# Kernel tuning notes

Measured on AMD Instinct MI355X. Metric: run time of the kernel, lower is better.

## Reference

```python
import jax, jax.numpy as jnp
import numpy as np

B, T = 128, 50
VOCAB, EMB_D, GRU_H = 10000, 200, 100
HEADS, AHID, THID = 8, 96, 96

def _conv(x, w, b, pad):
    y = jax.lax.conv_general_dilated(x, w, (1, 1), pad,
        dimension_numbers=('NCHW', 'OIHW', 'NCHW'))
    return y + b[None, :, None, None]

def _bn(x, g, b, m, v):
    s = jax.lax.rsqrt(v + 1e-5)
    return (x - m[None, :, None, None]) * (g * s)[None, :, None, None] + b[None, :, None, None]

def _maxpool(x):
    return jax.lax.reduce_window(x, -jnp.inf, jax.lax.max, (1, 1, 2, 2), (1, 1, 2, 2), 'VALID')

def _resize(x):
    # F.interpolate(mode='bilinear', align_corners=False) == half-pixel bilinear, no antialias
    return jax.image.resize(x, (x.shape[0], x.shape[1], 25, 156), 'bilinear', antialias=False)

def _audio_attn(x, wq, bq, wk, bk, wv, bv):
    # x: [B,96,H,W]; wq: [heads,96,96] == stacked per-head 1x1 convs
    Q = jnp.einsum('bchw,noc->bnohw', x, wq) + bq[None, :, :, None, None]
    K = jnp.einsum('bchw,noc->bnohw', x, wk) + bk[None, :, :, None, None]
    V = jnp.einsum('bchw,noc->bnohw', x, wv) + bv[None, :, :, None, None]
    # torch F.softmax with no dim on a 4D tensor defaults to dim=1 (channels) -> axis=2 here
    return jax.nn.softmax(Q * K, axis=2) * V  # [B,heads,96,H,W]

def _text_attn(o, wq, bq, wk, bk, wv, bv):
    # o: [N,100]; wq: [heads,96,100] == stacked per-head Linear layers
    Q = jnp.einsum('nd,hod->nho', o, wq) + bq[None]
    K = jnp.einsum('nd,hod->nho', o, wk) + bk[None]
    V = jnp.einsum('nd,hod->nho', o, wv) + bv[None]
    a = jax.nn.softmax(Q * K, axis=2) * V  # 2D softmax default dim=1 -> over feature axis
    return a.reshape(o.shape[0], -1)  # head-concat order == torch cat along dim=1

def _gru(xs, w_ih, w_hh, b_ih, b_hh):
    # xs: [T,B,200]; torch gate order r, z, n; b_hn applied inside r-gating
    def step(h, x):
        gi = x @ w_ih.T + b_ih
        gh = h @ w_hh.T + b_hh
        ir, iz, inew = jnp.split(gi, 3, axis=1)
        hr, hz, hnew = jnp.split(gh, 3, axis=1)
        r = jax.nn.sigmoid(ir + hr)
        z = jax.nn.sigmoid(iz + hz)
        n = jnp.tanh(inew + r * hnew)
        h2 = (1.0 - z) * n + z * h
        return h2, h2
    h0 = jnp.zeros((xs.shape[1], GRU_H), xs.dtype)
    hT, outs = jax.lax.scan(step, h0, xs)
    return outs, hT

def _forward(tokens, lengths, mfcc_t, mfcc_f, mfcc_c, w1a, b1a, g1a, be1a, m1a, v1a, w1b, b1b, g1b, be1b, m1b, v1b, w2, b2, g2, be2, m2, v2, w3, b3, g3, be3, m3, v3, w4, b4, g4, be4, m4, v4, wq_a1, bq_a1, wk_a1, bk_a1, wv_a1, bv_a1, wq_a2, bq_a2, wk_a2, bk_a2, wv_a2, bv_a2, emb, w_ih, w_hh, b_ih, b_hh, wq_t1, bq_t1, wk_t1, bk_t1, wv_t1, bv_t1, wq_t2, bq_t2, wk_t2, bk_t2, wv_t2, bv_t2, w_fa, b_fa, w_ft, b_ft, w_e, b_e):
    # --- audio CNN stem (eval-mode batchnorm; dropout off) ---
    xa = jax.nn.relu(_bn(_conv(mfcc_t, w1a, b1a, 'VALID'), g1a, be1a, m1a, v1a))
    xb = jax.nn.relu(_bn(_conv(mfcc_f, w1b, b1b, 'VALID'), g1b, be1b, m1b, v1b))
    # NOTE: original source reuses conv1b/bn1b for the third input (faithful to that)
    xc = jax.nn.relu(_bn(_conv(mfcc_c, w1b, b1b, 'VALID'), g1b, be1b, m1b, v1b))
    x = jnp.concatenate([_resize(xa), _resize(xb), _resize(xc)], axis=1)  # [B,24,25,156]
    x = _maxpool(jax.nn.relu(_bn(_conv(x, w2, b2, [(1, 1), (1, 1)]), g2, be2, m2, v2)))  # [B,32,12,78]
    x = _maxpool(jax.nn.relu(_bn(_conv(x, w3, b3, [(1, 1), (1, 1)]), g3, be3, m3, v3)))  # [B,64,6,39]
    x = jax.nn.relu(_bn(_conv(x, w4, b4, [(1, 1), (1, 1)]), g4, be4, m4, v4))            # [B,96,6,39]
    # --- two stacked per-head audio attentions, then per-head spatial GAP ---
    a1 = _audio_attn(x, wq_a1, bq_a1, wk_a1, bk_a1, wv_a1, bv_a1).mean(axis=(-2, -1))  # [B,8,96]
    a2 = _audio_attn(x, wq_a2, bq_a2, wk_a2, bk_a2, wv_a2, bv_a2).mean(axis=(-2, -1))
    # forward() slices heads along the height concat and GAPs -> per head [stage1 96, stage2 96]
    self_attn_audio = jnp.concatenate([a1, a2], axis=2).reshape(x.shape[0], -1)  # [B,1536]
    # --- text branch: embedding + GRU (all lengths == T -> pack/pad is identity) ---
    ex = jnp.swapaxes(emb[tokens], 0, 1)  # [T,B,200]
    outs, h = _gru(ex, w_ih, w_hh, b_ih, b_hh)  # h: [B,100]
    output = jnp.swapaxes(outs, 0, 1).reshape(-1, GRU_H)  # [B*T,100]
    t1 = _text_attn(output, wq_t1, bq_t1, wk_t1, bk_t1, wv_t1, bv_t1)
    t2 = _text_attn(output, wq_t2, bq_t2, wk_t2, bk_t2, wv_t2, bv_t2)
    self_attn_text = jnp.concatenate([t1, t2], axis=1).reshape(x.shape[0], T, -1).sum(axis=1)  # [B,1536]
    # --- cross-modal gated fusion ---
    x_gap = x.mean(axis=(-2, -1))  # [B,96]
    a_text = jax.nn.softmax(x_gap @ w_fa.T + b_fa, axis=1)   # [B,100]
    attn_text_based_audio = a_text * h                        # [B,100]
    a_audio = jax.nn.softmax(h @ w_ft.T + b_ft, axis=1)      # [B,96]
    attn_audio_based_text = a_audio * x_gap                   # [B,96]
    feat = jnp.concatenate([self_attn_audio, self_attn_text,
                            attn_audio_based_text, attn_text_based_audio], axis=1)  # [B,3268]
    return feat @ w_e.T + b_e  # [B,4] emotion logits

def setup_inputs() -> dict:
    key = jax.random.key(0)
    ks = iter(jax.random.split(key, 100))
    nrm = lambda s, sc=0.05: jax.random.normal(next(ks), s, jnp.float32) * sc
    uni = lambda s: jax.random.uniform(next(ks), s, jnp.float32) * 0.5 + 0.5
    d = {}
    d['mfcc_t'] = jax.random.normal(next(ks), (B, 1, 200, 40), jnp.float32)
    d['mfcc_f'] = jax.random.normal(next(ks), (B, 1, 200, 40), jnp.float32)
    d['mfcc_c'] = jax.random.normal(next(ks), (B, 1, 200, 40), jnp.float32)
    d['tokens'] = jax.random.randint(next(ks), (B, T), 0, VOCAB)
    d['lengths'] = jnp.full((B,), T, jnp.int32)
    def bnp(pre, c):
        d['g' + pre] = 1.0 + nrm((c,)); d['be' + pre] = nrm((c,))
        d['m' + pre] = nrm((c,)); d['v' + pre] = uni((c,))
    d['w1a'] = nrm((8, 1, 5, 2), 0.2); d['b1a'] = nrm((8,)); bnp('1a', 8)
    d['w1b'] = nrm((8, 1, 2, 6), 0.2); d['b1b'] = nrm((8,)); bnp('1b', 8)
    d['w2'] = nrm((32, 24, 3, 3), 0.1); d['b2'] = nrm((32,)); bnp('2', 32)
    d['w3'] = nrm((64, 32, 3, 3), 0.1); d['b3'] = nrm((64,)); bnp('3', 64)
    d['w4'] = nrm((96, 64, 3, 3), 0.08); d['b4'] = nrm((96,)); bnp('4', 96)
    for s in ('1', '2'):
        for p in ('q', 'k', 'v'):
            d['w%s_a%s' % (p, s)] = nrm((HEADS, 96, 96), 0.1)
            d['b%s_a%s' % (p, s)] = nrm((HEADS, 96))
    d['emb'] = nrm((VOCAB, EMB_D), 0.1)
    d['w_ih'] = nrm((3 * GRU_H, EMB_D), 0.1); d['w_hh'] = nrm((3 * GRU_H, GRU_H), 0.1)
    d['b_ih'] = nrm((3 * GRU_H,)); d['b_hh'] = nrm((3 * GRU_H,))
    for s in ('1', '2'):
        for p in ('q', 'k', 'v'):
            d['w%s_t%s' % (p, s)] = nrm((HEADS, THID, GRU_H), 0.1)
            d['b%s_t%s' % (p, s)] = nrm((HEADS, THID))
    d['w_fa'] = nrm((100, 96), 0.1); d['b_fa'] = nrm((100,))
    d['w_ft'] = nrm((96, 100), 0.1); d['b_ft'] = nrm((96,))
    d['w_e'] = nrm((4, 2 * HEADS * AHID + 2 * HEADS * THID + 96 + 100), 0.05); d['b_e'] = nrm((4,))
    return d

def reference(mfcc_t, mfcc_f, mfcc_c, tokens, lengths, w1a, b1a, g1a, be1a, m1a, v1a, w1b, b1b, g1b, be1b, m1b, v1b, w2, b2, g2, be2, m2, v2, w3, b3, g3, be3, m3, v3, w4, b4, g4, be4, m4, v4, wq_a1, bq_a1, wk_a1, bk_a1, wv_a1, bv_a1, wq_a2, bq_a2, wk_a2, bk_a2, wv_a2, bv_a2, emb, w_ih, w_hh, b_ih, b_hh, wq_t1, bq_t1, wk_t1, bk_t1, wv_t1, bv_t1, wq_t2, bq_t2, wk_t2, bk_t2, wv_t2, bv_t2, w_fa, b_fa, w_ft, b_ft, w_e, b_e):
    return _forward(tokens, lengths, mfcc_t, mfcc_f, mfcc_c, w1a, b1a, g1a, be1a, m1a, v1a, w1b, b1b, g1b, be1b, m1b, v1b, w2, b2, g2, be2, m2, v2, w3, b3, g3, be3, m3, v3, w4, b4, g4, be4, m4, v4, wq_a1, bq_a1, wk_a1, bk_a1, wv_a1, bv_a1, wq_a2, bq_a2, wk_a2, bk_a2, wv_a2, bv_a2, emb, w_ih, w_hh, b_ih, b_hh, wq_t1, bq_t1, wk_t1, bk_t1, wv_t1, bv_t1, wq_t2, bq_t2, wk_t2, bk_t2, wv_t2, bv_t2, w_fa, b_fa, w_ft, b_ft, w_e, b_e)
```

## Files before the change

kernel.cpp:

```cpp
#include <hip/hip_runtime.h>
#include <math.h>

static constexpr int kB = 128;
static constexpr int kT = 50;

struct TDesc { const float* src; float* dst; int O; int C; int total; };
struct TPack { TDesc d[15]; };
__global__ void k_transpose_pack(TPack p) {
    TDesc t = p.d[blockIdx.y];
    int idx = blockIdx.x * 256 + threadIdx.x;
    if (idx >= t.total) return;
    int o = idx % t.O; int r = idx / t.O; int c = r % t.C; int n = r / t.C;
    t.dst[idx] = t.src[((size_t)n * t.O + o) * t.C + c];
}

__global__ void k_zero(float* __restrict__ a, int n) {
    int i = blockIdx.x * 256 + threadIdx.x;
    if (i < n) a[i] = 0.f;
}

__global__ void k_stem(const float* __restrict__ mt, const float* __restrict__ mf,
                       const float* __restrict__ mc,
                       const float* __restrict__ w1a, const float* __restrict__ b1a,
                       const float* __restrict__ g1a, const float* __restrict__ be1a,
                       const float* __restrict__ m1a, const float* __restrict__ v1a,
                       const float* __restrict__ w1b, const float* __restrict__ b1b,
                       const float* __restrict__ g1b, const float* __restrict__ be1b,
                       const float* __restrict__ m1b, const float* __restrict__ v1b,
                       float* __restrict__ out, int total) {
    int idx = blockIdx.x * blockDim.x + threadIdx.x;
    if (idx >= total) return;
    int ox = idx % 156; int t = idx / 156;
    int oy = t % 25; t /= 25;
    int ch = t % 24; int b = t / 24;
    int grp = ch >> 3, c = ch & 7;
    const float* src; int Hc, Wc;
    const float *wb, *cb, *g, *be, *m, *v;
    if (grp == 0) { src = mt; Hc = 196; Wc = 39; wb = w1a + c * 10;
                    cb = b1a; g = g1a; be = be1a; m = m1a; v = v1a; }
    else          { src = (grp == 1 ? mf : mc); Hc = 199; Wc = 35; wb = w1b + c * 12;
                    cb = b1b; g = g1b; be = be1b; m = m1b; v = v1b; }
    float s = g[c] * rsqrtf(v[c] + 1e-5f);
    float bias = (cb[c] - m[c]) * s + be[c];
    float sy = (oy + 0.5f) * ((float)Hc / 25.f) - 0.5f;
    float sx = (ox + 0.5f) * ((float)Wc / 156.f) - 0.5f;
    float fy0 = floorf(sy), fx0 = floorf(sx);
    float fy = sy - fy0, fx = sx - fx0;
    int y0 = (int)fy0, x0 = (int)fx0;
    int y0c = min(max(y0, 0), Hc - 1), y1c = min(max(y0 + 1, 0), Hc - 1);
    int x0c = min(max(x0, 0), Wc - 1), x1c = min(max(x0 + 1, 0), Wc - 1);
    bool xs = (x1c == x0c), ys = (y1c == y0c);
    const float* p = src + (size_t)b * 8000;
    float t00, t01, t10, t11;
    if (grp == 0) {
        float W[6][3];
        #pragma unroll
        for (int r = 0; r < 6; ++r) {
            int rr = min(y0c + r, 199);
            #pragma unroll
            for (int cc = 0; cc < 3; ++cc)
                W[r][cc] = p[rr * 40 + min(x0c + cc, 39)];
        }
        float a00 = 0.f, a01 = 0.f, a10 = 0.f, a11 = 0.f;
        #pragma unroll
        for (int ky = 0; ky < 5; ++ky)
            #pragma unroll
            for (int kx = 0; kx < 2; ++kx) {
                float wv = wb[ky * 2 + kx];
                a00 += W[ky][kx] * wv;     a01 += W[ky][kx + 1] * wv;
                a10 += W[ky + 1][kx] * wv; a11 += W[ky + 1][kx + 1] * wv;
            }
        t00 = a00;
        t01 = xs ? a00 : a01;
        t10 = ys ? a00 : a10;
        t11 = xs ? (ys ? a00 : a10) : (ys ? a01 : a11);
    } else {
        float W[3][7];
        #pragma unroll
        for (int r = 0; r < 3; ++r) {
            int rr = min(y0c + r, 199);
            #pragma unroll
            for (int cc = 0; cc < 7; ++cc)
                W[r][cc] = p[rr * 40 + min(x0c + cc, 39)];
        }
        float a00 = 0.f, a01 = 0.f, a10 = 0.f, a11 = 0.f;
        #pragma unroll
        for (int ky = 0; ky < 2; ++ky)
            #pragma unroll
            for (int kx = 0; kx < 6; ++kx) {
                float wv = wb[ky * 6 + kx];
                a00 += W[ky][kx] * wv;     a01 += W[ky][kx + 1] * wv;
                a10 += W[ky + 1][kx] * wv; a11 += W[ky + 1][kx + 1] * wv;
            }
        t00 = a00;
        t01 = xs ? a00 : a01;
        t10 = ys ? a00 : a10;
        t11 = xs ? (ys ? a00 : a10) : (ys ? a01 : a11);
    }
    float r00 = fmaxf(t00 * s + bias, 0.f), r01 = fmaxf(t01 * s + bias, 0.f);
    float r10 = fmaxf(t10 * s + bias, 0.f), r11 = fmaxf(t11 * s + bias, 0.f);
    out[idx] = r00 * (1.f - fy) * (1.f - fx) + r01 * (1.f - fy) * fx
             + r10 * fy * (1.f - fx) + r11 * fy * fx;
}

template<int CIN, int CI_T, int H, int W, int ROWS, int NPX>
__global__ void __launch_bounds__(256) k_conv3x3_tiled(
    const float* __restrict__ in, const float* __restrict__ wT,
    const float* __restrict__ cb, const float* __restrict__ g,
    const float* __restrict__ be, const float* __restrict__ m,
    const float* __restrict__ v, float* __restrict__ out, int COUT) {
    constexpr int WP = W + 2;
    constexpr int RP = ROWS + 2;
    constexpr int STAGE = CI_T * RP * WP;
    __shared__ float sx[STAGE];
    __shared__ float sw[CI_T * 9 * 8];
    const int b = blockIdx.x, rt = blockIdx.y, oc0 = blockIdx.z * 8;
    const int row0 = rt * ROWS;
    const int tid = threadIdx.x;

    int off[NPX]; bool val[NPX];
    #pragma unroll
    for (int j = 0; j < NPX; ++j) {
        int px = tid + j * 256;
        int oy = px / W, ox = px - oy * W;
        bool ok = (px < ROWS * W) && (row0 + oy < H);
        val[j] = ok;
        off[j] = ok ? (oy * WP + ox) : 0;
    }

    float acc[NPX][8];
    #pragma unroll
    for (int j = 0; j < NPX; ++j)
        #pragma unroll
        for (int o = 0; o < 8; ++o) acc[j][o] = 0.f;

    for (int c0 = 0; c0 < CIN; c0 += CI_T) {
        __syncthreads();
        for (int e = tid; e < STAGE; e += 256) {
            int ci = e / (RP * WP);
            int rem = e - ci * RP * WP;
            int r = rem / WP;
            int xx = rem - r * WP;
            int iy = row0 - 1 + r;
            int ix = xx - 1;
            float vv = 0.f;
            if (iy >= 0 && iy < H && ix >= 0 && ix < W)
                vv = in[((size_t)(b * CIN + c0 + ci) * H + iy) * W + ix];
            sx[e] = vv;
        }
        for (int e = tid; e < CI_T * 9 * 8; e += 256) {
            int rk = e >> 3;
            int o = e & 7;
            sw[e] = wT[((size_t)c0 * 9 + rk) * COUT + oc0 + o];
        }
        __syncthreads();
        #pragma unroll 1
        for (int cl = 0; cl < CI_T; ++cl) {
            const float* sxc = sx + cl * RP * WP;
            #pragma unroll
            for (int k = 0; k < 9; ++k) {
                const int ky = k / 3, kx = k % 3;
                const float4 wa = *(const float4*)(sw + (cl * 9 + k) * 8);
                const float4 wb = *(const float4*)(sw + (cl * 9 + k) * 8 + 4);
                #pragma unroll
                for (int j = 0; j < NPX; ++j) {
                    float xv = sxc[off[j] + ky * WP + kx];
                    acc[j][0] += xv * wa.x; acc[j][1] += xv * wa.y;
                    acc[j][2] += xv * wa.z; acc[j][3] += xv * wa.w;
                    acc[j][4] += xv * wb.x; acc[j][5] += xv * wb.y;
                    acc[j][6] += xv * wb.z; acc[j][7] += xv * wb.w;
                }
            }
        }
    }
    float sc[8], bi[8];
    #pragma unroll
    for (int o = 0; o < 8; ++o) {
        float s = g[oc0 + o] * rsqrtf(v[oc0 + o] + 1e-5f);
        sc[o] = s; bi[o] = (cb[oc0 + o] - m[oc0 + o]) * s + be[oc0 + o];
    }
    #pragma unroll
    for (int j = 0; j < NPX; ++j) if (val[j]) {
        int px = tid + j * 256;
        int oy = row0 + px / W, ox = px % W;
        #pragma unroll
        for (int o = 0; o < 8; ++o)
            out[((size_t)(b * COUT + oc0 + o) * H + oy) * W + ox] =
                fmaxf(acc[j][o] * sc[o] + bi[o], 0.f);
    }
}

__global__ void k_maxpool(const float* __restrict__ in, float* __restrict__ out,
                          int C, int Hin, int Win, int Hout, int Wout, int total) {
    int idx = blockIdx.x * blockDim.x + threadIdx.x;
    if (idx >= total) return;
    int ox = idx % Wout; int t = idx / Wout;
    int oy = t % Hout; t /= Hout;
    int c = t % C; int b = t / C;
    const float* p = in + ((size_t)(b * C + c) * Hin + 2 * oy) * Win + 2 * ox;
    float m0 = fmaxf(p[0], p[1]);
    float m1 = fmaxf(p[Win], p[Win + 1]);
    out[idx] = fmaxf(m0, m1);
}

__global__ void __launch_bounds__(256) k_xgap(const float* __restrict__ x,
                                              float* __restrict__ xgap) {
    int b = blockIdx.x, tid = threadIdx.x;
    int wave = tid >> 6, lane = tid & 63;
    for (int c = wave; c < 96; c += 4) {
        const float* row = x + ((size_t)b * 96 + c) * 234;
        float s = 0.f;
        for (int p = lane; p < 234; p += 64) s += row[p];
        #pragma unroll
        for (int off = 1; off < 64; off <<= 1) s += __shfl_xor(s, off);
        if (lane == 0) xgap[b * 96 + c] = s * (1.f / 234.f);
    }
}

__global__ void __launch_bounds__(256, 2) k_audio_attn(
    const float* __restrict__ x,
    const float* __restrict__ wq1, const float* __restrict__ bq1,
    const float* __restrict__ wk1, const float* __restrict__ bk1,
    const float* __restrict__ wv1, const float* __restrict__ bv1,
    const float* __restrict__ wq2, const float* __restrict__ bq2,
    const float* __restrict__ wk2, const float* __restrict__ bk2,
    const float* __restrict__ wv2, const float* __restrict__ bv2,
    float* __restrict__ afeat) {
    const int b = blockIdx.x >> 1, pt = blockIdx.x & 1;
    const int n = blockIdx.y, stage = blockIdx.z;
    const float* wq = (stage ? wq2 : wq1) + n * 9216;
    const float* wk = (stage ? wk2 : wk1) + n * 9216;
    const float* wv = (stage ? wv2 : wv1) + n * 9216;
    const float* bqn = (stage ? bq2 : bq1) + n * 96;
    const float* bkn = (stage ? bk2 : bk1) + n * 96;
    const float* bvn = (stage ? bv2 : bv1) + n * 96;
    const int tid = threadIdx.x;
    const int to = tid >> 4, tpg = tid & 15;
    const int ob = to * 6;
    const int pA = tpg * 4;
    const int p0 = pt * 128;

    __shared__ float sxc[16 * 128];
    __shared__ float sw[4608];
    float* sred = sw;

    const float* xb = x + (size_t)b * (96 * 234) + p0;

    float qa[6][8], ka[6][8], va[6][8];
    #pragma unroll
    for (int j = 0; j < 6; ++j) {
        float bq_ = bqn[ob + j], bk_ = bkn[ob + j], bv_ = bvn[ob + j];
        #pragma unroll
        for (int i = 0; i < 8; ++i) { qa[j][i] = bq_; ka[j][i] = bk_; va[j][i] = bv_; }
    }

    for (int c0 = 0; c0 < 96; c0 += 16) {
        __syncthreads();
        {
            #pragma unroll
            for (int it = 0; it < 4; ++it) {
                int e2 = tid + it * 256;
                int r = e2 >> 6, c2 = (e2 & 63) * 2;
                float2 v = make_float2(0.f, 0.f);
                if (p0 + c2 < 234) v = *(const float2*)(xb + (c0 + r) * 234 + c2);
                *(float2*)(sxc + r * 128 + c2) = v;
            }
        }
        for (int e4 = tid; e4 < 1152; e4 += 256) {
            int mat = (e4 >= 768) ? 2 : (e4 >= 384 ? 1 : 0);
            int r4 = e4 - mat * 384;
            const float* wsrc = (mat == 0) ? wq : (mat == 1 ? wk : wv);
            *(float4*)(sw + mat * 1536 + r4 * 4) = *(const float4*)(wsrc + c0 * 96 + r4 * 4);
        }
        __syncthreads();
        #pragma unroll 2
        for (int cc = 0; cc < 16; ++cc) {
            float4 xa = *(const float4*)(sxc + cc * 128 + pA);
            float4 xc = *(const float4*)(sxc + cc * 128 + 64 + pA);
            const float* wr = sw + cc * 96 + ob;
            float2 q01 = *(const float2*)(wr);
            float2 q23 = *(const float2*)(wr + 2);
            float2 q45 = *(const float2*)(wr + 4);
            float2 k01 = *(const float2*)(wr + 1536);
            float2 k23 = *(const float2*)(wr + 1538);
            float2 k45 = *(const float2*)(wr + 1540);
            float2 v01 = *(const float2*)(wr + 3072);
            float2 v23 = *(const float2*)(wr + 3074);
            float2 v45 = *(const float2*)(wr + 3076);
            float wqv[6] = {q01.x, q01.y, q23.x, q23.y, q45.x, q45.y};
            float wkv[6] = {k01.x, k01.y, k23.x, k23.y, k45.x, k45.y};
            float wvv[6] = {v01.x, v01.y, v23.x, v23.y, v45.x, v45.y};
            #pragma unroll
            for (int j = 0; j < 6; ++j) {
                qa[j][0] += wqv[j] * xa.x; qa[j][1] += wqv[j] * xa.y;
                qa[j][2] += wqv[j] * xa.z; qa[j][3] += wqv[j] * xa.w;
                qa[j][4] += wqv[j] * xc.x; qa[j][5] += wqv[j] * xc.y;
                qa[j][6] += wqv[j] * xc.z; qa[j][7] += wqv[j] * xc.w;
                ka[j][0] += wkv[j] * xa.x; ka[j][1] += wkv[j] * xa.y;
                ka[j][2] += wkv[j] * xa.z; ka[j][3] += wkv[j] * xa.w;
                ka[j][4] += wkv[j] * xc.x; ka[j][5] += wkv[j] * xc.y;
                ka[j][6] += wkv[j] * xc.z; ka[j][7] += wkv[j] * xc.w;
                va[j][0] += wvv[j] * xa.x; va[j][1] += wvv[j] * xa.y;
                va[j][2] += wvv[j] * xa.z; va[j][3] += wvv[j] * xa.w;
                va[j][4] += wvv[j] * xc.x; va[j][5] += wvv[j] * xc.y;
                va[j][6] += wvv[j] * xc.z; va[j][7] += wvv[j] * xc.w;
            }
        }
    }

    int col[8];
    #pragma unroll
    for (int i = 0; i < 4; ++i) { col[i] = pA + i; col[4 + i] = 64 + pA + i; }

    float pmx[8];
    #pragma unroll
    for (int i = 0; i < 8; ++i) pmx[i] = -1e30f;
    #pragma unroll
    for (int j = 0; j < 6; ++j)
        #pragma unroll
        for (int i = 0; i < 8; ++i) {
            float sv = qa[j][i] * ka[j][i];
            qa[j][i] = sv;
            pmx[i] = fmaxf(pmx[i], sv);
        }
    __syncthreads();
    #pragma unroll
    for (int i = 0; i < 8; ++i) sred[to * 128 + col[i]] = pmx[i];
    __syncthreads();
    float m_[8];
    #pragma unroll
    for (int i = 0; i < 8; ++i) {
        float mm = -1e30f;
        for (int t = 0; t < 16; ++t) mm = fmaxf(mm, sred[t * 128 + col[i]]);
        m_[i] = mm;
    }
    __syncthreads();
    float z[8];
    #pragma unroll
    for (int i = 0; i < 8; ++i) z[i] = 0.f;
    #pragma unroll
    for (int j = 0; j < 6; ++j)
        #pragma unroll
        for (int i = 0; i < 8; ++i) {
            float e = __expf(qa[j][i] - m_[i]);
            qa[j][i] = e;
            z[i] += e;
        }
    #pragma unroll
    for (int i = 0; i < 8; ++i) sred[to * 128 + col[i]] = z[i];
    __syncthreads();
    float rz[8];
    #pragma unroll
    for (int i = 0; i < 8; ++i) {
        float zs = 0.f;
        for (int t = 0; t < 16; ++t) zs += sred[t * 128 + col[i]];
        rz[i] = (p0 + col[i] < 234) ? 1.f / zs : 0.f;
    }
    __syncthreads();
    #pragma unroll
    for (int j = 0; j < 6; ++j) {
        float po = 0.f;
        #pragma unroll
        for (int i = 0; i < 8; ++i) po += qa[j][i] * rz[i] * va[j][i];
        sred[(ob + j) * 16 + tpg] = po;
    }
    __syncthreads();
    if (tid < 96) {
        float ssum = 0.f;
        #pragma unroll
        for (int t = 0; t < 16; ++t) ssum += sred[tid * 16 + t];
        atomicAdd(afeat + b * 1536 + n * 192 + stage * 96 + tid, ssum * (1.f / 234.f));
    }
}

__global__ void __launch_bounds__(320) k_gi(const int* __restrict__ tokens,
        const float* __restrict__ emb, const float* __restrict__ w_ih,
        const float* __restrict__ b_ih, float* __restrict__ GI) {
    int r0 = blockIdx.x * 8;
    int tid = threadIdx.x;
    __shared__ float er[8][200];
    for (int e = tid; e < 1600; e += 320) {
        int r = e / 200, c = e - r * 200;
        er[r][c] = emb[(size_t)tokens[r0 + r] * 200 + c];
    }
    __syncthreads();
    if (tid < 300) {
        float acc[8];
        float bv = b_ih[tid];
        #pragma unroll
        for (int r = 0; r < 8; ++r) acc[r] = bv;
        for (int k4 = 0; k4 < 50; ++k4) {
            float4 w4 = *(const float4*)(w_ih + (size_t)tid * 200 + k4 * 4);
            #pragma unroll
            for (int r = 0; r < 8; ++r) {
                float4 x4 = *(const float4*)&er[r][k4 * 4];
                acc[r] += w4.x * x4.x + w4.y * x4.y + w4.z * x4.z + w4.w * x4.w;
            }
        }
        #pragma unroll
        for (int r = 0; r < 8; ++r)
            GI[(size_t)(r0 + r) * 300 + tid] = acc[r];
    }
}

__global__ void __launch_bounds__(320) k_gru_all(const float* __restrict__ GI,
        const float* __restrict__ w_hh, const float* __restrict__ b_hh,
        float* __restrict__ outs) {
    int b = blockIdx.x, tid = threadIdx.x;
    __shared__ float hs[100];
    __shared__ float gH[300];
    float4 wreg[25];
    float bias = 0.f;
    if (tid < 300) {
        bias = b_hh[tid];
        #pragma unroll
        for (int k4 = 0; k4 < 25; ++k4)
            wreg[k4] = *(const float4*)(w_hh + (size_t)tid * 100 + k4 * 4);
    }
    if (tid < 100) hs[tid] = 0.f;
    __syncthreads();
    for (int t = 0; t < kT; ++t) {
        if (tid < 300) {
            float gh = bias;
            #pragma unroll
            for (int k4 = 0; k4 < 25; ++k4) {
                float4 h4 = *(const float4*)&hs[k4 * 4];
                gh += wreg[k4].x * h4.x + wreg[k4].y * h4.y
                    + wreg[k4].z * h4.z + wreg[k4].w * h4.w;
            }
            gH[tid] = gh;
        }
        __syncthreads();
        if (tid < 100) {
            const float* gi = GI + ((size_t)b * kT + t) * 300;
            float r = 1.f / (1.f + expf(-(gi[tid] + gH[tid])));
            float z = 1.f / (1.f + expf(-(gi[100 + tid] + gH[100 + tid])));
            float nn = tanhf(gi[200 + tid] + r * gH[200 + tid]);
            float h2 = (1.f - z) * nn + z * hs[tid];
            hs[tid] = h2;
            outs[((size_t)b * kT + t) * 100 + tid] = h2;
        }
        __syncthreads();
    }
}

__global__ void __launch_bounds__(128) k_text_attn(const float* __restrict__ outs,
    const float* __restrict__ wq1, const float* __restrict__ bq1,
    const float* __restrict__ wk1, const float* __restrict__ bk1,
    const float* __restrict__ wv1, const float* __restrict__ bv1,
    const float* __restrict__ wq2, const float* __restrict__ bq2,
    const float* __restrict__ wk2, const float* __restrict__ bk2,
    const float* __restrict__ wv2, const float* __restrict__ bv2,
    float* __restrict__ tfeat) {
    int b = blockIdx.x, stage = blockIdx.y, n = blockIdx.z;
    const float* wq = stage ? wq2 : wq1; const float* bq = stage ? bq2 : bq1;
    const float* wk = stage ? wk2 : wk1; const float* bk = stage ? bk2 : bk1;
    const float* wv = stage ? wv2 : wv1; const float* bv = stage ? bv2 : bv1;
    int tid = threadIdx.x;
    bool act = tid < 96;
    int oo = act ? tid : 0;
    const float* wqc = wq + n * 9600 + oo;
    const float* wkc = wk + n * 9600 + oo;
    const float* wvc = wv + n * 9600 + oo;
    float bqv = act ? bq[n * 96 + tid] : 0.f;
    float bkv = act ? bk[n * 96 + tid] : 0.f;
    float bvv = act ? bv[n * 96 + tid] : 0.f;
    __shared__ float rows[10][100];
    __shared__ float wredM[2][10], wredS[2][10];
    float acc = 0.f;
    int wave = tid >> 6, lane = tid & 63;
    for (int tile = 0; tile < 5; ++tile) {
        int t0 = tile * 10;
        __syncthreads();
        for (int e = tid; e < 1000; e += 128) {
            int tt = e / 100, c = e - tt * 100;
            rows[tt][c] = outs[((size_t)b * kT + t0 + tt) * 100 + c];
        }
        __syncthreads();
        float q[10], k[10], v[10];
        #pragma unroll
        for (int tt = 0; tt < 10; ++tt) { q[tt] = bqv; k[tt] = bkv; v[tt] = bvv; }
        for (int c4 = 0; c4 < 25; ++c4) {
            int cb = c4 * 4 * 96;
            float q0 = wqc[cb], q1 = wqc[cb + 96], q2 = wqc[cb + 192], q3 = wqc[cb + 288];
            float k0 = wkc[cb], k1 = wkc[cb + 96], k2 = wkc[cb + 192], k3 = wkc[cb + 288];
            float v0 = wvc[cb], v1 = wvc[cb + 96], v2 = wvc[cb + 192], v3 = wvc[cb + 288];
            #pragma unroll
            for (int tt = 0; tt < 10; ++tt) {
                float4 x4 = *(const float4*)&rows[tt][c4 * 4];
                q[tt] += q0 * x4.x + q1 * x4.y + q2 * x4.z + q3 * x4.w;
                k[tt] += k0 * x4.x + k1 * x4.y + k2 * x4.z + k3 * x4.w;
                v[tt] += v0 * x4.x + v1 * x4.y + v2 * x4.z + v3 * x4.w;
            }
        }
        float s[10], e_[10];
        #pragma unroll
        for (int tt = 0; tt < 10; ++tt) s[tt] = act ? q[tt] * k[tt] : -1e30f;
        #pragma unroll
        for (int tt = 0; tt < 10; ++tt) {
            float m = s[tt];
            #pragma unroll
            for (int off = 1; off < 64; off <<= 1) m = fmaxf(m, __shfl_xor(m, off));
            if (lane == 0) wredM[wave][tt] = m;
        }
        __syncthreads();
        #pragma unroll
        for (int tt = 0; tt < 10; ++tt) {
            float mx = fmaxf(wredM[0][tt], wredM[1][tt]);
            e_[tt] = expf(s[tt] - mx);
        }
        #pragma unroll
        for (int tt = 0; tt < 10; ++tt) {
            float sm = e_[tt];
            #pragma unroll
            for (int off = 1; off < 64; off <<= 1) sm += __shfl_xor(sm, off);
            if (lane == 0) wredS[wave][tt] = sm;
        }
        __syncthreads();
        #pragma unroll
        for (int tt = 0; tt < 10; ++tt) {
            float sm = wredS[0][tt] + wredS[1][tt];
            acc += e_[tt] / sm * v[tt];
        }
    }
    if (act) tfeat[b * 1536 + stage * 768 + n * 96 + tid] = acc;
}

__global__ void __launch_bounds__(128) k_final(const float* __restrict__ xgap,
    const float* __restrict__ outs, const float* __restrict__ afeat,
    const float* __restrict__ tfeat,
    const float* __restrict__ w_fa, const float* __restrict__ b_fa,
    const float* __restrict__ w_ft, const float* __restrict__ b_ft,
    const float* __restrict__ w_e, const float* __restrict__ b_e,
    float* __restrict__ out) {
    int b = blockIdx.x; int tid = threadIdx.x;
    __shared__ float xg[96], hv[100], st[100], sa[96], aat[96], atba[100];
    __shared__ float redm[2], reds[2];
    if (tid < 96) xg[tid] = xgap[b * 96 + tid];
    if (tid < 100) hv[tid] = outs[(size_t)(b * kT + kT - 1) * 100 + tid];
    __syncthreads();
    if (tid < 100) {
        float acc = b_fa[tid];
        const float* wr = w_fa + tid * 96;
        for (int c = 0; c < 96; ++c) acc += wr[c] * xg[c];
        st[tid] = acc;
    }
    if (tid < 96) {
        float acc = b_ft[tid];
        const float* wr = w_ft + tid * 100;
        for (int c = 0; c < 100; ++c) acc += wr[c] * hv[c];
        sa[tid] = acc;
    }
    __syncthreads();
    if (tid == 0) {
        float mxv = -1e30f; for (int i = 0; i < 100; ++i) mxv = fmaxf(mxv, st[i]);
        float s = 0.f; for (int i = 0; i < 100; ++i) s += expf(st[i] - mxv);
        redm[0] = mxv; reds[0] = s;
    }
    if (tid == 1) {
        float mxv = -1e30f; for (int i = 0; i < 96; ++i) mxv = fmaxf(mxv, sa[i]);
        float s = 0.f; for (int i = 0; i < 96; ++i) s += expf(sa[i] - mxv);
        redm[1] = mxv; reds[1] = s;
    }
    __syncthreads();
    if (tid < 100) atba[tid] = expf(st[tid] - redm[0]) / reds[0] * hv[tid];
    if (tid < 96)  aat[tid]  = expf(sa[tid] - redm[1]) / reds[1] * xg[tid];
    __syncthreads();
    float a0 = 0.f, a1 = 0.f, a2 = 0.f, a3 = 0.f;
    for (int col = tid; col < 3268; col += 128) {
        float f;
        if (col < 1536)      f = afeat[b * 1536 + col];
        else if (col < 3072) f = tfeat[b * 1536 + col - 1536];
        else if (col < 3168) f = aat[col - 3072];
        else                 f = atba[col - 3168];
        a0 += w_e[col] * f;            a1 += w_e[3268 + col] * f;
        a2 += w_e[2 * 3268 + col] * f; a3 += w_e[3 * 3268 + col] * f;
    }
    __shared__ float r4[4][128];
    r4[0][tid] = a0; r4[1][tid] = a1; r4[2][tid] = a2; r4[3][tid] = a3;
    __syncthreads();
    if (tid < 4) {
        float s = 0.f;
        for (int i = 0; i < 128; ++i) s += r4[tid][i];
        out[b * 4 + tid] = s + b_e[tid];
    }
}

extern "C" void kernel_launch(void* const* d_in, const int* in_sizes, int n_in,
                              void* d_out, int out_size, void* d_ws, size_t ws_size,
                              hipStream_t stream) {
    (void)in_sizes; (void)n_in; (void)out_size; (void)ws_size;
    const float* mfcc_t = (const float*)d_in[0];
    const float* mfcc_f = (const float*)d_in[1];
    const float* mfcc_c = (const float*)d_in[2];
    const int*   tokens = (const int*)d_in[3];
    const float *w1a = (const float*)d_in[5],  *b1a = (const float*)d_in[6],
                *g1a = (const float*)d_in[7],  *be1a = (const float*)d_in[8],
                *m1a = (const float*)d_in[9],  *v1a = (const float*)d_in[10];
    const float *w1b = (const float*)d_in[11], *b1b = (const float*)d_in[12],
                *g1b = (const float*)d_in[13], *be1b = (const float*)d_in[14],
                *m1b = (const float*)d_in[15], *v1b = (const float*)d_in[16];
    const float *w2 = (const float*)d_in[17], *b2 = (const float*)d_in[18],
                *g2 = (const float*)d_in[19], *be2 = (const float*)d_in[20],
                *m2 = (const float*)d_in[21], *v2 = (const float*)d_in[22];
    const float *w3 = (const float*)d_in[23], *b3 = (const float*)d_in[24],
                *g3 = (const float*)d_in[25], *be3 = (const float*)d_in[26],
                *m3 = (const float*)d_in[27], *v3 = (const float*)d_in[28];
    const float *w4 = (const float*)d_in[29], *b4 = (const float*)d_in[30],
                *g4 = (const float*)d_in[31], *be4 = (const float*)d_in[32],
                *m4 = (const float*)d_in[33], *v4 = (const float*)d_in[34];
    const float *wq_a1 = (const float*)d_in[35], *bq_a1 = (const float*)d_in[36],
                *wk_a1 = (const float*)d_in[37], *bk_a1 = (const float*)d_in[38],
                *wv_a1 = (const float*)d_in[39], *bv_a1 = (const float*)d_in[40];
    const float *wq_a2 = (const float*)d_in[41], *bq_a2 = (const float*)d_in[42],
                *wk_a2 = (const float*)d_in[43], *bk_a2 = (const float*)d_in[44],
                *wv_a2 = (const float*)d_in[45], *bv_a2 = (const float*)d_in[46];
    const float *emb  = (const float*)d_in[47];
    const float *w_ih = (const float*)d_in[48], *w_hh = (const float*)d_in[49],
                *b_ih = (const float*)d_in[50], *b_hh = (const float*)d_in[51];
    const float *wq_t1 = (const float*)d_in[52], *bq_t1 = (const float*)d_in[53],
                *wk_t1 = (const float*)d_in[54], *bk_t1 = (const float*)d_in[55],
                *wv_t1 = (const float*)d_in[56], *bv_t1 = (const float*)d_in[57];
    const float *wq_t2 = (const float*)d_in[58], *bq_t2 = (const float*)d_in[59],
                *wk_t2 = (const float*)d_in[60], *bk_t2 = (const float*)d_in[61],
                *wv_t2 = (const float*)d_in[62], *bv_t2 = (const float*)d_in[63];
    const float *w_fa = (const float*)d_in[64], *b_fa = (const float*)d_in[65],
                *w_ft = (const float*)d_in[66], *b_ft = (const float*)d_in[67],
                *w_e  = (const float*)d_in[68], *b_e  = (const float*)d_in[69];

    float* ws = (float*)d_ws;
    const size_t Z0 = 0;
    const size_t Z1 = 22091776ull;
    const size_t OUTS  = 34072576ull;
    const size_t AFEAT = 34712576ull;
    const size_t TFEAT = 34909184ull;
    const size_t XGAP  = 35105792ull;
    const size_t WT    = 35118080ull;
    float* X1 = ws + Z1;
    float* C2 = ws + Z0;  float* P2 = ws + Z1;
    float* C3 = ws + Z0;  float* P3 = ws + Z1;
    float* X4 = ws + Z0;  float* GI = ws + Z1;
    float* outs  = ws + OUTS;
    float* afeat = ws + AFEAT;
    float* tfeat = ws + TFEAT;
    float* xgap  = ws + XGAP;
    float* wqa1t = ws + WT;
    float* wka1t = wqa1t + 73728; float* wva1t = wka1t + 73728;
    float* wqa2t = wva1t + 73728; float* wka2t = wqa2t + 73728; float* wva2t = wka2t + 73728;
    float* wqt1t = wva2t + 73728;
    float* wkt1t = wqt1t + 76800; float* wvt1t = wkt1t + 76800;
    float* wqt2t = wvt1t + 76800; float* wkt2t = wqt2t + 76800; float* wvt2t = wkt2t + 76800;
    float* wT2 = outs;
    float* wT3 = outs + 6912;
    float* wT4 = outs + 25344;

    TPack tp;
    tp.d[0]  = {wq_a1, wqa1t, 96, 96, 73728};
    tp.d[1]  = {wk_a1, wka1t, 96, 96, 73728};
    tp.d[2]  = {wv_a1, wva1t, 96, 96, 73728};
    tp.d[3]  = {wq_a2, wqa2t, 96, 96, 73728};
    tp.d[4]  = {wk_a2, wka2t, 96, 96, 73728};
    tp.d[5]  = {wv_a2, wva2t, 96, 96, 73728};
    tp.d[6]  = {w2, wT2, 32, 216, 6912};
    tp.d[7]  = {w3, wT3, 64, 288, 18432};
    tp.d[8]  = {w4, wT4, 96, 576, 55296};
    tp.d[9]  = {wq_t1, wqt1t, 96, 100, 76800};
    tp.d[10] = {wk_t1, wkt1t, 96, 100, 76800};
    tp.d[11] = {wv_t1, wvt1t, 96, 100, 76800};
    tp.d[12] = {wq_t2, wqt2t, 96, 100, 76800};
    tp.d[13] = {wk_t2, wkt2t, 96, 100, 76800};
    tp.d[14] = {wv_t2, wvt2t, 96, 100, 76800};
    k_transpose_pack<<<dim3(300, 15), 256, 0, stream>>>(tp);

    k_zero<<<768, 256, 0, stream>>>(afeat, 196608);

    k_stem<<<46800, 256, 0, stream>>>(mfcc_t, mfcc_f, mfcc_c,
        w1a, b1a, g1a, be1a, m1a, v1a,
        w1b, b1b, g1b, be1b, m1b, v1b, X1, 11980800);
    k_conv3x3_tiled<24, 8, 25, 156, 9, 6><<<dim3(128, 3, 4), 256, 0, stream>>>(
        X1, wT2, b2, g2, be2, m2, v2, C2, 32);
    k_maxpool<<<14976, 256, 0, stream>>>(C2, P2, 32, 25, 156, 12, 78, 3833856);
    k_conv3x3_tiled<32, 8, 12, 78, 12, 4><<<dim3(128, 1, 8), 256, 0, stream>>>(
        P2, wT3, b3, g3, be3, m3, v3, C3, 64);
    k_maxpool<<<7488, 256, 0, stream>>>(C3, P3, 64, 12, 78, 6, 39, 1916928);
    k_conv3x3_tiled<64, 16, 6, 39, 6, 1><<<dim3(128, 1, 12), 256, 0, stream>>>(
        P3, wT4, b4, g4, be4, m4, v4, X4, 96);

    k_xgap<<<kB, 256, 0, stream>>>(X4, xgap);

    k_audio_attn<<<dim3(kB * 2, 8, 2), 256, 0, stream>>>(X4,
        wqa1t, bq_a1, wka1t, bk_a1, wva1t, bv_a1,
        wqa2t, bq_a2, wka2t, bk_a2, wva2t, bv_a2, afeat);

    k_gi<<<kB * kT / 8, 320, 0, stream>>>(tokens, emb, w_ih, b_ih, GI);
    k_gru_all<<<kB, 320, 0, stream>>>(GI, w_hh, b_hh, outs);
    k_text_attn<<<dim3(kB, 2, 8), 128, 0, stream>>>(outs,
        wqt1t, bq_t1, wkt1t, bk_t1, wvt1t, bv_t1,
        wqt2t, bq_t2, wkt2t, bk_t2, wvt2t, bv_t2, tfeat);

    k_final<<<kB, 128, 0, stream>>>(xgap, outs, afeat, tfeat,
                                    w_fa, b_fa, w_ft, b_ft, w_e, b_e, (float*)d_out);
}
```

Measured before the change: 1.418 ms.

## Fuse GRU recurrence into stem kernel blocks and fold zeroing into transpose

The sequential GRU recurrence now runs as the first 128 blocks of the stem kernel, so the long latency-bound scan overlaps with the massively parallel stem work instead of running serially after the conv chain. GI is computed before the stem and workspace buffers are remapped to avoid aliasing. The afeat zeroing moves into an extra grid row of the transpose kernel, removing one launch. The GRU blocks now run with 256 threads and read w_hh from global or cache each step instead of holding it in registers, which may slow the recurrence itself.

```diff
diff --git a/kernel.cpp b/kernel.cpp
--- a/kernel.cpp
+++ b/kernel.cpp
@@ -6,7 +6,12 @@
 
 struct TDesc { const float* src; float* dst; int O; int C; int total; };
 struct TPack { TDesc d[15]; };
-__global__ void k_transpose_pack(TPack p) {
+__global__ void k_transpose_pack(TPack p, float* __restrict__ za) {
+    if (blockIdx.y == 15) {
+        for (int i = blockIdx.x * 256 + threadIdx.x; i < 196608; i += 76800)
+            za[i] = 0.f;
+        return;
+    }
     TDesc t = p.d[blockIdx.y];
     int idx = blockIdx.x * 256 + threadIdx.x;
     if (idx >= t.total) return;
@@ -14,21 +19,94 @@
     t.dst[idx] = t.src[((size_t)n * t.O + o) * t.C + c];
 }
 
-__global__ void k_zero(float* __restrict__ a, int n) {
-    int i = blockIdx.x * 256 + threadIdx.x;
-    if (i < n) a[i] = 0.f;
-}
-
-__global__ void k_stem(const float* __restrict__ mt, const float* __restrict__ mf,
-                       const float* __restrict__ mc,
-                       const float* __restrict__ w1a, const float* __restrict__ b1a,
-                       const float* __restrict__ g1a, const float* __restrict__ be1a,
-                       const float* __restrict__ m1a, const float* __restrict__ v1a,
-                       const float* __restrict__ w1b, const float* __restrict__ b1b,
-                       const float* __restrict__ g1b, const float* __restrict__ be1b,
-                       const float* __restrict__ m1b, const float* __restrict__ v1b,
-                       float* __restrict__ out, int total) {
-    int idx = blockIdx.x * blockDim.x + threadIdx.x;
+__global__ void __launch_bounds__(320) k_gi(const int* __restrict__ tokens,
+        const float* __restrict__ emb, const float* __restrict__ w_ih,
+        const float* __restrict__ b_ih, float* __restrict__ GI) {
+    int r0 = blockIdx.x * 8;
+    int tid = threadIdx.x;
+    __shared__ float er[8][200];
+    for (int e = tid; e < 1600; e += 320) {
+        int r = e / 200, c = e - r * 200;
+        er[r][c] = emb[(size_t)tokens[r0 + r] * 200 + c];
+    }
+    __syncthreads();
+    if (tid < 300) {
+        float acc[8];
+        float bv = b_ih[tid];
+        #pragma unroll
+        for (int r = 0; r < 8; ++r) acc[r] = bv;
+        for (int k4 = 0; k4 < 50; ++k4) {
+            float4 w4 = *(const float4*)(w_ih + (size_t)tid * 200 + k4 * 4);
+            #pragma unroll
+            for (int r = 0; r < 8; ++r) {
+                float4 x4 = *(const float4*)&er[r][k4 * 4];
+                acc[r] += w4.x * x4.x + w4.y * x4.y + w4.z * x4.z + w4.w * x4.w;
+            }
+        }
+        #pragma unroll
+        for (int r = 0; r < 8; ++r)
+            GI[(size_t)(r0 + r) * 300 + tid] = acc[r];
+    }
+}
+
+__global__ void __launch_bounds__(256) k_fat_stem_gru(
+    const float* __restrict__ mt, const float* __restrict__ mf,
+    const float* __restrict__ mc,
+    const float* __restrict__ w1a, const float* __restrict__ b1a,
+    const float* __restrict__ g1a, const float* __restrict__ be1a,
+    const float* __restrict__ m1a, const float* __restrict__ v1a,
+    const float* __restrict__ w1b, const float* __restrict__ b1b,
+    const float* __restrict__ g1b, const float* __restrict__ be1b,
+    const float* __restrict__ m1b, const float* __restrict__ v1b,
+    float* __restrict__ out, int total,
+    const float* __restrict__ GI, const float* __restrict__ w_hh,
+    const float* __restrict__ b_hh, float* __restrict__ outs) {
+    if (blockIdx.x < 128) {
+        const int b = blockIdx.x, tid = threadIdx.x;
+        __shared__ float hs[100];
+        __shared__ float gH[300];
+        const float bias0 = b_hh[tid];
+        const float bias1 = (tid < 44) ? b_hh[256 + tid] : 0.f;
+        if (tid < 100) hs[tid] = 0.f;
+        __syncthreads();
+        for (int t = 0; t < kT; ++t) {
+            {
+                float gh = bias0;
+                const float* wr = w_hh + (size_t)tid * 100;
+                #pragma unroll
+                for (int k4 = 0; k4 < 25; ++k4) {
+                    float4 w4 = *(const float4*)(wr + k4 * 4);
+                    float4 h4 = *(const float4*)&hs[k4 * 4];
+                    gh += w4.x * h4.x + w4.y * h4.y + w4.z * h4.z + w4.w * h4.w;
+                }
+                gH[tid] = gh;
+            }
+            if (tid < 44) {
+                float gh = bias1;
+                const float* wr = w_hh + (size_t)(256 + tid) * 100;
+                #pragma unroll
+                for (int k4 = 0; k4 < 25; ++k4) {
+                    float4 w4 = *(const float4*)(wr + k4 * 4);
+                    float4 h4 = *(const float4*)&hs[k4 * 4];
+                    gh += w4.x * h4.x + w4.y * h4.y + w4.z * h4.z + w4.w * h4.w;
+                }
+                gH[256 + tid] = gh;
+            }
+            __syncthreads();
+            if (tid < 100) {
+                const float* gi = GI + ((size_t)b * kT + t) * 300;
+                float r = 1.f / (1.f + expf(-(gi[tid] + gH[tid])));
+                float z = 1.f / (1.f + expf(-(gi[100 + tid] + gH[100 + tid])));
+                float nn = tanhf(gi[200 + tid] + r * gH[200 + tid]);
+                float h2 = (1.f - z) * nn + z * hs[tid];
+                hs[tid] = h2;
+                outs[((size_t)b * kT + t) * 100 + tid] = h2;
+            }
+            __syncthreads();
+        }
+        return;
+    }
+    int idx = (blockIdx.x - 128) * 256 + threadIdx.x;
     if (idx >= total) return;
     int ox = idx % 156; int t = idx / 156;
     int oy = t % 25; t /= 25;
@@ -370,77 +448,6 @@
         #pragma unroll
         for (int t = 0; t < 16; ++t) ssum += sred[tid * 16 + t];
         atomicAdd(afeat + b * 1536 + n * 192 + stage * 96 + tid, ssum * (1.f / 234.f));
-    }
-}
-
-__global__ void __launch_bounds__(320) k_gi(const int* __restrict__ tokens,
-        const float* __restrict__ emb, const float* __restrict__ w_ih,
-        const float* __restrict__ b_ih, float* __restrict__ GI) {
-    int r0 = blockIdx.x * 8;
-    int tid = threadIdx.x;
-    __shared__ float er[8][200];
-    for (int e = tid; e < 1600; e += 320) {
-        int r = e / 200, c = e - r * 200;
-        er[r][c] = emb[(size_t)tokens[r0 + r] * 200 + c];
-    }
-    __syncthreads();
-    if (tid < 300) {
-        float acc[8];
-        float bv = b_ih[tid];
-        #pragma unroll
-        for (int r = 0; r < 8; ++r) acc[r] = bv;
-        for (int k4 = 0; k4 < 50; ++k4) {
-            float4 w4 = *(const float4*)(w_ih + (size_t)tid * 200 + k4 * 4);
-            #pragma unroll
-            for (int r = 0; r < 8; ++r) {
-                float4 x4 = *(const float4*)&er[r][k4 * 4];
-                acc[r] += w4.x * x4.x + w4.y * x4.y + w4.z * x4.z + w4.w * x4.w;
-            }
-        }
-        #pragma unroll
-        for (int r = 0; r < 8; ++r)
-            GI[(size_t)(r0 + r) * 300 + tid] = acc[r];
-    }
-}
-
-__global__ void __launch_bounds__(320) k_gru_all(const float* __restrict__ GI,
-        const float* __restrict__ w_hh, const float* __restrict__ b_hh,
-        float* __restrict__ outs) {
-    int b = blockIdx.x, tid = threadIdx.x;
-    __shared__ float hs[100];
-    __shared__ float gH[300];
-    float4 wreg[25];
-    float bias = 0.f;
-    if (tid < 300) {
-        bias = b_hh[tid];
-        #pragma unroll
-        for (int k4 = 0; k4 < 25; ++k4)
-            wreg[k4] = *(const float4*)(w_hh + (size_t)tid * 100 + k4 * 4);
-    }
-    if (tid < 100) hs[tid] = 0.f;
-    __syncthreads();
-    for (int t = 0; t < kT; ++t) {
-        if (tid < 300) {
-            float gh = bias;
-            #pragma unroll
-            for (int k4 = 0; k4 < 25; ++k4) {
-                float4 h4 = *(const float4*)&hs[k4 * 4];
-                gh += wreg[k4].x * h4.x + wreg[k4].y * h4.y
-                    + wreg[k4].z * h4.z + wreg[k4].w * h4.w;
-            }
-            gH[tid] = gh;
-        }
-        __syncthreads();
-        if (tid < 100) {
-            const float* gi = GI + ((size_t)b * kT + t) * 300;
-            float r = 1.f / (1.f + expf(-(gi[tid] + gH[tid])));
-            float z = 1.f / (1.f + expf(-(gi[100 + tid] + gH[100 + tid])));
-            float nn = tanhf(gi[200 + tid] + r * gH[200 + tid]);
-            float h2 = (1.f - z) * nn + z * hs[tid];
-            hs[tid] = h2;
-            outs[((size_t)b * kT + t) * 100 + tid] = h2;
-        }
-        __syncthreads();
     }
 }
 
@@ -636,10 +643,11 @@
     const size_t TFEAT = 34909184ull;
     const size_t XGAP  = 35105792ull;
     const size_t WT    = 35118080ull;
+    float* GI = ws + Z0;
     float* X1 = ws + Z1;
     float* C2 = ws + Z0;  float* P2 = ws + Z1;
     float* C3 = ws + Z0;  float* P3 = ws + Z1;
-    float* X4 = ws + Z0;  float* GI = ws + Z1;
+    float* X4 = ws + Z0;
     float* outs  = ws + OUTS;
     float* afeat = ws + AFEAT;
     float* tfeat = ws + TFEAT;
@@ -650,9 +658,9 @@
     float* wqt1t = wva2t + 73728;
     float* wkt1t = wqt1t + 76800; float* wvt1t = wkt1t + 76800;
     float* wqt2t = wvt1t + 76800; float* wkt2t = wqt2t + 76800; float* wvt2t = wkt2t + 76800;
-    float* wT2 = outs;
-    float* wT3 = outs + 6912;
-    float* wT4 = outs + 25344;
+    float* wT2 = tfeat;
+    float* wT3 = tfeat + 6912;
+    float* wT4 = tfeat + 25344;
 
     TPack tp;
     tp.d[0]  = {wq_a1, wqa1t, 96, 96, 73728};
@@ -670,13 +678,15 @@
     tp.d[12] = {wq_t2, wqt2t, 96, 100, 76800};
     tp.d[13] = {wk_t2, wkt2t, 96, 100, 76800};
     tp.d[14] = {wv_t2, wvt2t, 96, 100, 76800};
-    k_transpose_pack<<<dim3(300, 15), 256, 0, stream>>>(tp);
-
-    k_zero<<<768, 256, 0, stream>>>(afeat, 196608);
-
-    k_stem<<<46800, 256, 0, stream>>>(mfcc_t, mfcc_f, mfcc_c,
+    k_transpose_pack<<<dim3(300, 16), 256, 0, stream>>>(tp, afeat);
+
+    k_gi<<<kB * kT / 8, 320, 0, stream>>>(tokens, emb, w_ih, b_ih, GI);
+
+    k_fat_stem_gru<<<46928, 256, 0, stream>>>(mfcc_t, mfcc_f, mfcc_c,
         w1a, b1a, g1a, be1a, m1a, v1a,
-        w1b, b1b, g1b, be1b, m1b, v1b, X1, 11980800);
+        w1b, b1b, g1b, be1b, m1b, v1b, X1, 11980800,
+        GI, w_hh, b_hh, outs);
+
     k_conv3x3_tiled<24, 8, 25, 156, 9, 6><<<dim3(128, 3, 4), 256, 0, stream>>>(
         X1, wT2, b2, g2, be2, m2, v2, C2, 32);
     k_maxpool<<<14976, 256, 0, stream>>>(C2, P2, 32, 25, 156, 12, 78, 3833856);
@@ -686,18 +696,15 @@
     k_conv3x3_tiled<64, 16, 6, 39, 6, 1><<<dim3(128, 1, 12), 256, 0, stream>>>(
         P3, wT4, b4, g4, be4, m4, v4, X4, 96);
 
+    k_text_attn<<<dim3(kB, 2, 8), 128, 0, stream>>>(outs,
+        wqt1t, bq_t1, wkt1t, bk_t1, wvt1t, bv_t1,
+        wqt2t, bq_t2, wkt2t, bk_t2, wvt2t, bv_t2, tfeat);
     k_xgap<<<kB, 256, 0, stream>>>(X4, xgap);
 
     k_audio_attn<<<dim3(kB * 2, 8, 2), 256, 0, stream>>>(X4,
         wqa1t, bq_a1, wka1t, bk_a1, wva1t, bv_a1,
         wqa2t, bq_a2, wka2t, bk_a2, wva2t, bv_a2, afeat);
 
-    k_gi<<<kB * kT / 8, 320, 0, stream>>>(tokens, emb, w_ih, b_ih, GI);
-    k_gru_all<<<kB, 320, 0, stream>>>(GI, w_hh, b_hh, outs);
-    k_text_attn<<<dim3(kB, 2, 8), 128, 0, stream>>>(outs,
-        wqt1t, bq_t1, wkt1t, bk_t1, wvt1t, bv_t1,
-        wqt2t, bq_t2, wkt2t, bk_t2, wvt2t, bv_t2, tfeat);
-
     k_final<<<kB, 128, 0, stream>>>(xgap, outs, afeat, tfeat,
                                     w_fa, b_fa, w_ft, b_ft, w_e, b_e, (float*)d_out);
 }
```

New measurement: 1.419 ms. Within noise of the previous version (+0.1%).
